# Performance work log

Hardware: AMD Instinct MI355X
Metric: run time of the kernel (lower is better)

## Reference

```python
import jax, jax.numpy as jnp
import numpy as np

N = 50000        # nodes
E_RAND = 800000  # random edges (self-loops appended)
H = 4            # heads
F_IN, D1, D2 = 128, 64, 64
MLP_H, NCLS = 200, 2
NEG_SLOPE = 0.2
EPS = 1e-5


def setup_inputs() -> dict:
    key = jax.random.key(0)
    ks = jax.random.split(key, 18)
    p = lambda k, shape: (jax.random.normal(k, shape, jnp.float32) * 0.05)
    features = jax.random.normal(ks[0], (N, F_IN), jnp.float32)
    loops = jnp.arange(N, dtype=jnp.int32)
    src = jnp.concatenate([jax.random.randint(ks[1], (E_RAND,), 0, N, jnp.int32), loops])
    dst = jnp.concatenate([jax.random.randint(ks[2], (E_RAND,), 0, N, jnp.int32), loops])
    return {
        "features": features, "src": src, "dst": dst,
        "W1": p(ks[3], (F_IN, H * D1)), "al1": p(ks[4], (H, D1)), "ar1": p(ks[5], (H, D1)), "b1": p(ks[6], (H * D1,)),
        "W2": p(ks[7], (D1, H * D2)), "al2": p(ks[8], (H, D2)), "ar2": p(ks[9], (H, D2)), "b2": p(ks[10], (H * D2,)),
        "Wm1": p(ks[11], (D2, MLP_H)), "bm1": p(ks[12], (MLP_H,)),
        "gamma": jnp.ones((MLP_H,), jnp.float32), "beta": jnp.zeros((MLP_H,), jnp.float32),
        "Wm2": p(ks[13], (MLP_H, NCLS)), "bm2": p(ks[14], (NCLS,)),
    }


def gat_layer(x, W, al, ar, b, src, dst):
    # x: [N, F]; W: [F, H*D]
    Hh, D = al.shape
    h = (x @ W).reshape(N, Hh, D)                      # [N,H,D]
    el = jnp.einsum('nhd,hd->nh', h, al)               # [N,H]
    er = jnp.einsum('nhd,hd->nh', h, ar)               # [N,H]
    e = jax.nn.leaky_relu(el[src] + er[dst], NEG_SLOPE)  # [E,H]
    # edge softmax over incoming edges of each dst node
    m = jax.ops.segment_max(e, dst, num_segments=N)    # [N,H]
    ex = jnp.exp(e - m[dst])
    s = jax.ops.segment_sum(ex, dst, num_segments=N)   # [N,H]
    a = ex / s[dst]                                    # [E,H]
    out = jax.ops.segment_sum(a[:, :, None] * h[src], dst, num_segments=N)  # [N,H,D]
    out = jax.nn.relu(out + b.reshape(1, Hh, D))
    return out.mean(axis=1)                            # mean over heads -> [N,D]


def reference(features, src, dst, W1, al1, ar1, b1, W2, al2, ar2, b2,
              Wm1, bm1, gamma, beta, Wm2, bm2):
    h = gat_layer(features, W1, al1, ar1, b1, src, dst)   # dropout = identity (eval)
    h = gat_layer(h, W2, al2, ar2, b2, src, dst)
    # MLPPredictor: Dropout(id) -> Linear -> ReLU -> BatchNorm1d (batch stats) -> Linear
    z = jax.nn.relu(h @ Wm1 + bm1)                        # [N, MLP_H]
    mu = z.mean(axis=0)
    var = ((z - mu) ** 2).mean(axis=0)                    # biased var (torch BN)
    z = (z - mu) * jax.lax.rsqrt(var + EPS) * gamma + beta
    return z @ Wm2 + bm2                                  # [N, NCLS]
```

## Files before the change

### kernel.cpp

```cpp
#include <hip/hip_runtime.h>
#include <hip/hip_bf16.h>

#define NNODES 50000
#define MLP_HID 200
#define NB_SCAN 196
#define CAP 128

#define NB_W1   256
#define NB_W2   256
#define NB_ZC   196
#define INIT_BLOCKS (NB_W1 + NB_W2 + NB_ZC + 1)

typedef __attribute__((ext_vector_type(8))) short bf16x8;
typedef __attribute__((ext_vector_type(4))) float f32x4;

__device__ __forceinline__ unsigned short f2bf(float x){
    unsigned u = __float_as_uint(x);
    unsigned r = (u + 0x7fffu + ((u >> 16) & 1u)) >> 16;
    return (unsigned short)r;
}
__device__ __forceinline__ float bflo(unsigned u){ return __uint_as_float(u << 16); }
__device__ __forceinline__ float bfhi(unsigned u){ return __uint_as_float(u & 0xffff0000u); }

__global__ __launch_bounds__(256) void init_all(
    const float* __restrict__ W1, unsigned short* __restrict__ W1T,
    const float* __restrict__ W2, unsigned short* __restrict__ W2T,
    int* __restrict__ cnt, float* __restrict__ bn_acc )
{
    const int b = blockIdx.x, tid = threadIdx.x;
    if (b < NB_W1){
        int c = b;
        if (tid < 128) W1T[(size_t)c * 128 + tid] = f2bf(W1[(size_t)tid * 256 + c]);
    } else if (b < NB_W1 + NB_W2){
        int c = b - NB_W1;
        if (tid < 64) W2T[(size_t)c * 64 + tid] = f2bf(W2[(size_t)tid * 256 + c]);
    } else if (b < NB_W1 + NB_W2 + NB_ZC){
        int i = (b - NB_W1 - NB_W2) * 256 + tid;
        if (i < NNODES) cnt[i] = 0;
    } else {
        if (tid < 2 * MLP_HID - 256) bn_acc[256 + tid] = 0.f;
        bn_acc[tid] = 0.f;
    }
}

template<int K, bool F32IN>
__global__ __launch_bounds__(256) void mfma_gemm_attn(
    const void* __restrict__ Aptr,
    const unsigned short* __restrict__ WT,
    const float* __restrict__ al, const float* __restrict__ ar,
    unsigned short* __restrict__ hb,
    float* __restrict__ el, float* __restrict__ er, int M)
{
    const int wv = threadIdx.x >> 6, lane = threadIdx.x & 63;
    const int r0 = blockIdx.x * 64 + wv * 16;
    const int l15 = lane & 15, ks = lane >> 4;

    f32x4 acc[16];
    #pragma unroll
    for (int nt = 0; nt < 16; nt++)
        #pragma unroll
        for (int q = 0; q < 4; q++) acc[nt][q] = 0.f;

    const int arow = min(r0 + l15, M - 1);
    const unsigned short* aptr_b = (const unsigned short*)Aptr + (size_t)arow * K + ks * 8;
    const float*          aptr_f = (const float*)Aptr          + (size_t)arow * K + ks * 8;
    const unsigned short* bptr = WT + (size_t)l15 * K + ks * 8;

    #pragma unroll
    for (int k0 = 0; k0 < K; k0 += 32){
        bf16x8 a;
        if (F32IN){
            float4 f0 = *(const float4*)(aptr_f + k0);
            float4 f1 = *(const float4*)(aptr_f + k0 + 4);
            a[0] = (short)f2bf(f0.x); a[1] = (short)f2bf(f0.y);
            a[2] = (short)f2bf(f0.z); a[3] = (short)f2bf(f0.w);
            a[4] = (short)f2bf(f1.x); a[5] = (short)f2bf(f1.y);
            a[6] = (short)f2bf(f1.z); a[7] = (short)f2bf(f1.w);
        } else {
            a = *(const bf16x8*)(aptr_b + k0);
        }
        #pragma unroll
        for (int nt = 0; nt < 16; nt++){
            bf16x8 b = *(const bf16x8*)(bptr + (size_t)nt * 16 * K + k0);
            acc[nt] = __builtin_amdgcn_mfma_f32_16x16x32_bf16(a, b, acc[nt], 0, 0, 0);
        }
    }

    float elv[4][4], erv[4][4];
    #pragma unroll
    for (int r = 0; r < 4; r++)
        #pragma unroll
        for (int hh = 0; hh < 4; hh++){ elv[r][hh] = 0.f; erv[r][hh] = 0.f; }

    #pragma unroll
    for (int nt = 0; nt < 16; nt++){
        int col = nt * 16 + l15;
        float alv = al[col], arv = ar[col];
        #pragma unroll
        for (int reg = 0; reg < 4; reg++){
            elv[reg][nt >> 2] = fmaf(acc[nt][reg], alv, elv[reg][nt >> 2]);
            erv[reg][nt >> 2] = fmaf(acc[nt][reg], arv, erv[reg][nt >> 2]);
        }
    }
    #pragma unroll
    for (int o = 8; o > 0; o >>= 1){
        #pragma unroll
        for (int reg = 0; reg < 4; reg++)
            #pragma unroll
            for (int hh = 0; hh < 4; hh++){
                elv[reg][hh] += __shfl_xor(elv[reg][hh], o);
                erv[reg][hh] += __shfl_xor(erv[reg][hh], o);
            }
    }
    if (l15 == 0){
        #pragma unroll
        for (int reg = 0; reg < 4; reg++){
            int r = r0 + ks * 4 + reg;
            if (r < M){
                #pragma unroll
                for (int hh = 0; hh < 4; hh++){
                    el[r * 4 + hh] = elv[reg][hh];
                    er[r * 4 + hh] = erv[reg][hh];
                }
            }
        }
    }

    __shared__ __align__(16) unsigned short hbuf[4][16][264];
    #pragma unroll
    for (int nt = 0; nt < 16; nt++)
        #pragma unroll
        for (int reg = 0; reg < 4; reg++)
            hbuf[wv][ks * 4 + reg][nt * 16 + l15] = f2bf(acc[nt][reg]);
    #pragma unroll
    for (int t = 0; t < 8; t++){
        int chunk = t * 64 + lane;
        int rr = chunk >> 5;
        int cc = (chunk & 31) * 8;
        int r = r0 + rr;
        if (r < M){
            uint4 v = *(const uint4*)&hbuf[wv][rr][cc];
            *(uint4*)&hb[(size_t)r * 256 + cc] = v;
        }
    }
}

template<int KT, bool RELU, bool BN>
__global__ __launch_bounds__(256) void gemm_tile(const float* __restrict__ A,
                                                 const float* __restrict__ B,
                                                 const float* __restrict__ bias,
                                                 float* __restrict__ C,
                                                 float* __restrict__ bn_sum,
                                                 float* __restrict__ bn_sumsq,
                                                 int M, int Nc){
    __shared__ float As[16][64];
    __shared__ float Bs[16][64];
    __shared__ float bnred[16][64];
    const int tid = threadIdx.x;
    const int tx = tid & 15, ty = tid >> 4;
    const int r0 = blockIdx.y * 64, c0 = blockIdx.x * 64;
    float acc[4][4] = {};
    const int lr  = tid >> 2,  lk4 = (tid & 3) * 4;
    const int bk  = tid >> 4,  bc4 = (tid & 15) * 4;

    for (int k0 = 0; k0 < KT; k0 += 16){
        float4 av = make_float4(0.f,0.f,0.f,0.f);
        if (r0 + lr < M) av = *(const float4*)&A[(size_t)(r0 + lr) * KT + k0 + lk4];
        As[lk4+0][lr] = av.x; As[lk4+1][lr] = av.y;
        As[lk4+2][lr] = av.z; As[lk4+3][lr] = av.w;

        if (c0 + bc4 + 3 < Nc){
            float4 bv = *(const float4*)&B[(size_t)(k0 + bk) * Nc + c0 + bc4];
            Bs[bk][bc4+0] = bv.x; Bs[bk][bc4+1] = bv.y;
            Bs[bk][bc4+2] = bv.z; Bs[bk][bc4+3] = bv.w;
        } else {
            #pragma unroll
            for (int j = 0; j < 4; j++){
                int c = c0 + bc4 + j;
                Bs[bk][bc4+j] = (c < Nc) ? B[(size_t)(k0 + bk) * Nc + c] : 0.f;
            }
        }
        __syncthreads();
        #pragma unroll
        for (int kk = 0; kk < 16; kk++){
            float4 a = *(const float4*)&As[kk][ty*4];
            float4 b = *(const float4*)&Bs[kk][tx*4];
            float arr[4] = {a.x,a.y,a.z,a.w};
            float brr[4] = {b.x,b.y,b.z,b.w};
            #pragma unroll
            for (int i = 0; i < 4; i++)
                #pragma unroll
                for (int j = 0; j < 4; j++)
                    acc[i][j] = fmaf(arr[i], brr[j], acc[i][j]);
        }
        __syncthreads();
    }

    float cs[4] = {0,0,0,0}, css[4] = {0,0,0,0};
    #pragma unroll
    for (int i = 0; i < 4; i++){
        int r = r0 + ty*4 + i;
        bool rok = r < M;
        #pragma unroll
        for (int j = 0; j < 4; j++){
            int c = c0 + tx*4 + j;
            if (c >= Nc) continue;
            float v = acc[i][j];
            if (bias) v += bias[c];
            if (RELU) v = fmaxf(v, 0.f);
            if (rok){
                C[(size_t)r * Nc + c] = v;
                if (BN){ cs[j] += v; css[j] += v * v; }
            }
        }
    }
    if (BN){
        #pragma unroll
        for (int j = 0; j < 4; j++) bnred[ty][tx*4+j] = cs[j];
        __syncthreads();
        if (tid < 64){
            float s = 0.f;
            #pragma unroll
            for (int t = 0; t < 16; t++) s += bnred[t][tid];
            if (c0 + tid < Nc) atomicAdd(&bn_sum[c0 + tid], s);
        }
        __syncthreads();
        #pragma unroll
        for (int j = 0; j < 4; j++) bnred[ty][tx*4+j] = css[j];
        __syncthreads();
        if (tid < 64){
            float s = 0.f;
            #pragma unroll
            for (int t = 0; t < 16; t++) s += bnred[t][tid];
            if (c0 + tid < Nc) atomicAdd(&bn_sumsq[c0 + tid], s);
        }
    }
}

__global__ __launch_bounds__(256) void csr_count(const int* __restrict__ dst,
                                                 int* __restrict__ cnt, int E){
    int e = blockIdx.x * blockDim.x + threadIdx.x;
    if (e < E) atomicAdd(&cnt[dst[e]], 1);
}

__global__ __launch_bounds__(256) void csr_bsum(const int* __restrict__ cnt,
                                                int* __restrict__ bsum){
    __shared__ int red[256];
    int i = blockIdx.x * 256 + threadIdx.x;
    red[threadIdx.x] = (i < NNODES) ? cnt[i] : 0;
    __syncthreads();
    for (int off = 128; off > 0; off >>= 1){
        if (threadIdx.x < off) red[threadIdx.x] += red[threadIdx.x + off];
        __syncthreads();
    }
    if (threadIdx.x == 0) bsum[blockIdx.x] = red[0];
}

__global__ __launch_bounds__(256) void csr_bscan(const int* __restrict__ bsum,
                                                 int* __restrict__ boff){
    __shared__ int part[256];
    int t = threadIdx.x;
    int v = (t < NB_SCAN) ? bsum[t] : 0;
    part[t] = v;
    __syncthreads();
    for (int off = 1; off < 256; off <<= 1){
        int u = (t >= off) ? part[t - off] : 0;
        __syncthreads();
        part[t] += u;
        __syncthreads();
    }
    if (t < NB_SCAN) boff[t] = part[t] - v;
}

__global__ __launch_bounds__(256) void csr_fill(const int* __restrict__ cnt,
                                                const int* __restrict__ boff,
                                                int* __restrict__ row_ptr,
                                                int* __restrict__ cursor){
    __shared__ int part[256];
    int b = blockIdx.x, t = threadIdx.x;
    int i = b * 256 + t;
    int c = (i < NNODES) ? cnt[i] : 0;
    part[t] = c;
    __syncthreads();
    for (int off = 1; off < 256; off <<= 1){
        int u = (t >= off) ? part[t - off] : 0;
        __syncthreads();
        part[t] += u;
        __syncthreads();
    }
    int excl = part[t] - c + boff[b];
    if (i < NNODES){ row_ptr[i] = excl; cursor[i] = excl; }
    if (i == NNODES - 1) row_ptr[NNODES] = excl + c;
}

__global__ __launch_bounds__(256) void csr_scatter(const int* __restrict__ src,
                                                   const int* __restrict__ dst,
                                                   int* __restrict__ cursor,
                                                   int* __restrict__ col_src, int E){
    int e = blockIdx.x * blockDim.x + threadIdx.x;
    if (e >= E) return;
    int pos = atomicAdd(&cursor[dst[e]], 1);
    col_src[pos] = src[e];
}

__global__ __launch_bounds__(256) void gat_edge_v7(
    const int* __restrict__ row_ptr, const int* __restrict__ col_src,
    const float* __restrict__ el, const float* __restrict__ er,
    const unsigned short* __restrict__ hb, const float* __restrict__ bias,
    float* __restrict__ out_f, unsigned short* __restrict__ out_b, int N)
{
    __shared__ float s_w[4][4][132];
    __shared__ int   s_idx[4][CAP];

    const int wv = threadIdx.x >> 6;
    const int lane = threadIdx.x & 63;
    const int n = blockIdx.x * 4 + wv;
    if (n >= N) return;

    const int rs = row_ptr[n], re = row_ptr[n + 1];
    const int K = re - rs;
    const float4 ern = *(const float4*)&er[n * 4];
    float (*sw)[132] = s_w[wv];
    int* sidx = s_idx[wv];

    float ls0 = 0.f, ls1 = 0.f, ls2 = 0.f, ls3 = 0.f;
    for (int k = lane; k < K; k += 64){
        int s = col_src[rs + k];
        float4 e4 = *(const float4*)&el[s * 4];
        float e0 = e4.x + ern.x; e0 = (e0 >= 0.f) ? e0 : 0.2f * e0;
        float e1 = e4.y + ern.y; e1 = (e1 >= 0.f) ? e1 : 0.2f * e1;
        float e2 = e4.z + ern.z; e2 = (e2 >= 0.f) ? e2 : 0.2f * e2;
        float e3 = e4.w + ern.w; e3 = (e3 >= 0.f) ? e3 : 0.2f * e3;
        float w0 = __expf(e0), w1 = __expf(e1), w2 = __expf(e2), w3 = __expf(e3);
        if (k < CAP){
            sidx[k] = s;
            sw[0][k] = w0; sw[1][k] = w1; sw[2][k] = w2; sw[3][k] = w3;
        }
        ls0 += w0; ls1 += w1; ls2 += w2; ls3 += w3;
    }
    #pragma unroll
    for (int o = 32; o > 0; o >>= 1){
        ls0 += __shfl_xor(ls0, o); ls1 += __shfl_xor(ls1, o);
        ls2 += __shfl_xor(ls2, o); ls3 += __shfl_xor(ls3, o);
    }
    const int slot = lane >> 5;
    const int c8   = (lane & 31) * 8;
    const int hc   = c8 >> 6;
    const float invh = 1.f / (hc == 0 ? ls0 : hc == 1 ? ls1 : hc == 2 ? ls2 : ls3);

    float acc[8];
    #pragma unroll
    for (int q = 0; q < 8; q++) acc[q] = 0.f;

    for (int base = 0; base < K; base += CAP){
        if (base > 0){
            for (int k = base + lane; k < min(K, base + CAP); k += 64){
                int s = col_src[rs + k];
                float4 e4 = *(const float4*)&el[s * 4];
                float e0 = e4.x + ern.x; e0 = (e0 >= 0.f) ? e0 : 0.2f * e0;
                float e1 = e4.y + ern.y; e1 = (e1 >= 0.f) ? e1 : 0.2f * e1;
                float e2 = e4.z + ern.z; e2 = (e2 >= 0.f) ? e2 : 0.2f * e2;
                float e3 = e4.w + ern.w; e3 = (e3 >= 0.f) ? e3 : 0.2f * e3;
                int kk = k - base;
                sidx[kk] = s;
                sw[0][kk] = __expf(e0); sw[1][kk] = __expf(e1);
                sw[2][kk] = __expf(e2); sw[3][kk] = __expf(e3);
            }
        }
        const int rem = min(CAP, K - base);
        for (int j = slot; j < rem; j += 8){
            int   j1 = j + 2, j2 = j + 4, j3 = j + 6;
            int   jc1 = min(j1, rem - 1), jc2 = min(j2, rem - 1), jc3 = min(j3, rem - 1);
            float w0v = sw[hc][j];
            float w1v = (j1 < rem) ? sw[hc][j1] : 0.f;
            float w2v = (j2 < rem) ? sw[hc][j2] : 0.f;
            float w3v = (j3 < rem) ? sw[hc][j3] : 0.f;
            int   s0 = sidx[j], s1 = sidx[jc1], s2 = sidx[jc2], s3 = sidx[jc3];
            uint4 v0 = *(const uint4*)&hb[(size_t)s0 * 256 + c8];
            uint4 v1 = *(const uint4*)&hb[(size_t)s1 * 256 + c8];
            uint4 v2 = *(const uint4*)&hb[(size_t)s2 * 256 + c8];
            uint4 v3 = *(const uint4*)&hb[(size_t)s3 * 256 + c8];
            acc[0] = fmaf(w0v, bflo(v0.x), acc[0]); acc[1] = fmaf(w0v, bfhi(v0.x), acc[1]);
            acc[2] = fmaf(w0v, bflo(v0.y), acc[2]); acc[3] = fmaf(w0v, bfhi(v0.y), acc[3]);
            acc[4] = fmaf(w0v, bflo(v0.z), acc[4]); acc[5] = fmaf(w0v, bfhi(v0.z), acc[5]);
            acc[6] = fmaf(w0v, bflo(v0.w), acc[6]); acc[7] = fmaf(w0v, bfhi(v0.w), acc[7]);
            acc[0] = fmaf(w1v, bflo(v1.x), acc[0]); acc[1] = fmaf(w1v, bfhi(v1.x), acc[1]);
            acc[2] = fmaf(w1v, bflo(v1.y), acc[2]); acc[3] = fmaf(w1v, bfhi(v1.y), acc[3]);
            acc[4] = fmaf(w1v, bflo(v1.z), acc[4]); acc[5] = fmaf(w1v, bfhi(v1.z), acc[5]);
            acc[6] = fmaf(w1v, bflo(v1.w), acc[6]); acc[7] = fmaf(w1v, bfhi(v1.w), acc[7]);
            acc[0] = fmaf(w2v, bflo(v2.x), acc[0]); acc[1] = fmaf(w2v, bfhi(v2.x), acc[1]);
            acc[2] = fmaf(w2v, bflo(v2.y), acc[2]); acc[3] = fmaf(w2v, bfhi(v2.y), acc[3]);
            acc[4] = fmaf(w2v, bflo(v2.z), acc[4]); acc[5] = fmaf(w2v, bfhi(v2.z), acc[5]);
            acc[6] = fmaf(w2v, bflo(v2.w), acc[6]); acc[7] = fmaf(w2v, bfhi(v2.w), acc[7]);
            acc[0] = fmaf(w3v, bflo(v3.x), acc[0]); acc[1] = fmaf(w3v, bfhi(v3.x), acc[1]);
            acc[2] = fmaf(w3v, bflo(v3.y), acc[2]); acc[3] = fmaf(w3v, bfhi(v3.y), acc[3]);
            acc[4] = fmaf(w3v, bflo(v3.z), acc[4]); acc[5] = fmaf(w3v, bfhi(v3.z), acc[5]);
            acc[6] = fmaf(w3v, bflo(v3.w), acc[6]); acc[7] = fmaf(w3v, bfhi(v3.w), acc[7]);
        }
    }

    #pragma unroll
    for (int q = 0; q < 8; q++){
        acc[q] *= invh;
        acc[q] += __shfl_xor(acc[q], 32);
        acc[q] = fmaxf(acc[q] + bias[c8 + q], 0.f);
        acc[q] += __shfl_xor(acc[q], 8);
        acc[q] += __shfl_xor(acc[q], 16);
        acc[q] *= 0.25f;
    }
    if (lane < 8){
        uint4 pb;
        pb.x = (unsigned)f2bf(acc[0]) | ((unsigned)f2bf(acc[1]) << 16);
        pb.y = (unsigned)f2bf(acc[2]) | ((unsigned)f2bf(acc[3]) << 16);
        pb.z = (unsigned)f2bf(acc[4]) | ((unsigned)f2bf(acc[5]) << 16);
        pb.w = (unsigned)f2bf(acc[6]) | ((unsigned)f2bf(acc[7]) << 16);
        *(uint4*)&out_b[(size_t)n * 64 + lane * 8] = pb;
        if (out_f){
            *(float4*)&out_f[(size_t)n * 64 + lane * 8]     = make_float4(acc[0], acc[1], acc[2], acc[3]);
            *(float4*)&out_f[(size_t)n * 64 + lane * 8 + 4] = make_float4(acc[4], acc[5], acc[6], acc[7]);
        }
    }
}

__global__ __launch_bounds__(256) void mlp2(const float* __restrict__ z,
                                            const float* __restrict__ bn_sum,
                                            const float* __restrict__ bn_sumsq,
                                            const float* __restrict__ gamma,
                                            const float* __restrict__ beta,
                                            const float* __restrict__ Wm2,
                                            const float* __restrict__ bm2,
                                            float* __restrict__ out,
                                            int Nrows){
    __shared__ float s_scale[MLP_HID], s_shift[MLP_HID];
    const int tid = threadIdx.x;
    if (tid < MLP_HID){
        float inv = 1.f / (float)Nrows;
        float mu = bn_sum[tid] * inv;
        float var = bn_sumsq[tid] * inv - mu * mu;
        float rstd = rsqrtf(var + 1e-5f);
        float sc = rstd * gamma[tid];
        s_scale[tid] = sc;
        s_shift[tid] = beta[tid] - mu * sc;
    }
    __syncthreads();
    int n = (blockIdx.x * 256 + tid) >> 6;
    if (n >= Nrows) return;
    int lane = tid & 63;
    float a0 = 0.f, a1 = 0.f;
    for (int k = lane; k < MLP_HID; k += 64){
        float zn = z[(size_t)n * MLP_HID + k] * s_scale[k] + s_shift[k];
        a0 = fmaf(zn, Wm2[k * 2 + 0], a0);
        a1 = fmaf(zn, Wm2[k * 2 + 1], a1);
    }
    #pragma unroll
    for (int o = 32; o > 0; o >>= 1){
        a0 += __shfl_xor(a0, o);
        a1 += __shfl_xor(a1, o);
    }
    if (lane == 0){
        out[n * 2 + 0] = a0 + bm2[0];
        out[n * 2 + 1] = a1 + bm2[1];
    }
}

extern "C" void kernel_launch(void* const* d_in, const int* in_sizes, int n_in,
                              void* d_out, int out_size, void* d_ws, size_t ws_size,
                              hipStream_t stream) {
    const float* feat  = (const float*)d_in[0];
    const int*   src   = (const int*)  d_in[1];
    const int*   dst   = (const int*)  d_in[2];
    const float* W1    = (const float*)d_in[3];
    const float* al1   = (const float*)d_in[4];
    const float* ar1   = (const float*)d_in[5];
    const float* b1    = (const float*)d_in[6];
    const float* W2    = (const float*)d_in[7];
    const float* al2   = (const float*)d_in[8];
    const float* ar2   = (const float*)d_in[9];
    const float* b2    = (const float*)d_in[10];
    const float* Wm1   = (const float*)d_in[11];
    const float* bm1   = (const float*)d_in[12];
    const float* gamma = (const float*)d_in[13];
    const float* beta  = (const float*)d_in[14];
    const float* Wm2   = (const float*)d_in[15];
    const float* bm2   = (const float*)d_in[16];
    const int E = in_sizes[1];
    float* out = (float*)d_out;

    unsigned short* h_bf   = (unsigned short*)d_ws;
    unsigned short* o1_bf  = h_bf   + (size_t)NNODES * 256;
    unsigned short* o2_bf  = o1_bf  + (size_t)NNODES * 64;
    unsigned short* W1T    = o2_bf  + (size_t)NNODES * 64;
    unsigned short* W2T    = W1T + 256 * 128;
    float* z      = (float*)(W2T + 256 * 64);
    float* out2_f = z      + (size_t)NNODES * MLP_HID;
    float* el     = out2_f + (size_t)NNODES * 64;
    float* er     = el     + (size_t)NNODES * 4;
    float* bn_sum   = er + (size_t)NNODES * 4;
    float* bn_sumsq = bn_sum + MLP_HID;
    int* cnt      = (int*)(bn_sumsq + MLP_HID);
    int* row_ptr  = cnt + NNODES;
    int* cursor   = row_ptr + NNODES + 1;
    int* bsum     = cursor + NNODES;
    int* boff     = bsum + 256;
    int* col_src  = boff + 256;

    const dim3 blk(256);
    const int eg = (E + 255) / 256;
    const int gb = (NNODES + 63) / 64;
    const int ng4 = (NNODES + 3) / 4;

    init_all<<<INIT_BLOCKS, blk, 0, stream>>>(W1, W1T, W2, W2T, cnt, bn_sum);

    csr_count<<<eg, blk, 0, stream>>>(dst, cnt, E);
    csr_bsum<<<NB_SCAN, blk, 0, stream>>>(cnt, bsum);
    csr_bscan<<<1, blk, 0, stream>>>(bsum, boff);
    csr_fill<<<NB_SCAN, blk, 0, stream>>>(cnt, boff, row_ptr, cursor);
    csr_scatter<<<eg, blk, 0, stream>>>(src, dst, cursor, col_src, E);

    mfma_gemm_attn<128, true><<<gb, blk, 0, stream>>>(feat, W1T, al1, ar1,
                                                      h_bf, el, er, NNODES);
    gat_edge_v7<<<ng4, blk, 0, stream>>>(row_ptr, col_src, el, er, h_bf, b1,
                                         nullptr, o1_bf, NNODES);

    mfma_gemm_attn<64, false><<<gb, blk, 0, stream>>>(o1_bf, W2T, al2, ar2,
                                                      h_bf, el, er, NNODES);
    gat_edge_v7<<<ng4, blk, 0, stream>>>(row_ptr, col_src, el, er, h_bf, b2,
                                         out2_f, o2_bf, NNODES);

    gemm_tile<64,true,true><<<dim3((MLP_HID + 63) / 64, gb), blk, 0, stream>>>(
        out2_f, Wm1, bm1, z, bn_sum, bn_sumsq, NNODES, MLP_HID);

    mlp2<<<(NNODES * 64 + 255) / 256, blk, 0, stream>>>(
        z, bn_sum, bn_sumsq, gamma, beta, Wm2, bm2, out, NNODES);
}
```

Measured before the change: 372.3 us.

## Split GAT edge kernel into weight pass and slab-sliced aggregation

The GEMM now writes node features into eight 64-byte feature slabs, each holding 8 dims across all heads, instead of 512-byte rows. Edge aggregation is split in two. A weight kernel precomputes normalized softmax weights per edge as packed bf16 and writes them to a new buffer. A slab kernel then gathers from one slice per block, so the gathered working set per pass is smaller and more cache-friendly. In exchange it adds an extra kernel launch and an edge-weight array write/read per layer, re-reads col_src eight times, and rounds the attention weights to bf16.

```diff
diff --git a/kernel.cpp b/kernel.cpp
--- a/kernel.cpp
+++ b/kernel.cpp
@@ -48,7 +48,7 @@
     const void* __restrict__ Aptr,
     const unsigned short* __restrict__ WT,
     const float* __restrict__ al, const float* __restrict__ ar,
-    unsigned short* __restrict__ hb,
+    unsigned short* __restrict__ hslab,
     float* __restrict__ el, float* __restrict__ er, int M)
 {
     const int wv = threadIdx.x >> 6, lane = threadIdx.x & 63;
@@ -139,8 +139,11 @@
         int cc = (chunk & 31) * 8;
         int r = r0 + rr;
         if (r < M){
+            int hh = cc >> 6;
+            int d0 = cc & 63;
+            int s  = d0 >> 3;
             uint4 v = *(const uint4*)&hbuf[wv][rr][cc];
-            *(uint4*)&hb[(size_t)r * 256 + cc] = v;
+            *(uint4*)&hslab[((size_t)s * NNODES + r) * 32 + hh * 8] = v;
         }
     }
 }
@@ -303,15 +306,12 @@
     col_src[pos] = src[e];
 }
 
-__global__ __launch_bounds__(256) void gat_edge_v7(
+__global__ __launch_bounds__(256) void gat_edge_wts(
     const int* __restrict__ row_ptr, const int* __restrict__ col_src,
     const float* __restrict__ el, const float* __restrict__ er,
-    const unsigned short* __restrict__ hb, const float* __restrict__ bias,
-    float* __restrict__ out_f, unsigned short* __restrict__ out_b, int N)
+    uint2* __restrict__ apack, int N)
 {
     __shared__ float s_w[4][4][132];
-    __shared__ int   s_idx[4][CAP];
-
     const int wv = threadIdx.x >> 6;
     const int lane = threadIdx.x & 63;
     const int n = blockIdx.x * 4 + wv;
@@ -321,7 +321,6 @@
     const int K = re - rs;
     const float4 ern = *(const float4*)&er[n * 4];
     float (*sw)[132] = s_w[wv];
-    int* sidx = s_idx[wv];
 
     float ls0 = 0.f, ls1 = 0.f, ls2 = 0.f, ls3 = 0.f;
     for (int k = lane; k < K; k += 64){
@@ -333,7 +332,6 @@
         float e3 = e4.w + ern.w; e3 = (e3 >= 0.f) ? e3 : 0.2f * e3;
         float w0 = __expf(e0), w1 = __expf(e1), w2 = __expf(e2), w3 = __expf(e3);
         if (k < CAP){
-            sidx[k] = s;
             sw[0][k] = w0; sw[1][k] = w1; sw[2][k] = w2; sw[3][k] = w3;
         }
         ls0 += w0; ls1 += w1; ls2 += w2; ls3 += w3;
@@ -343,81 +341,83 @@
         ls0 += __shfl_xor(ls0, o); ls1 += __shfl_xor(ls1, o);
         ls2 += __shfl_xor(ls2, o); ls3 += __shfl_xor(ls3, o);
     }
-    const int slot = lane >> 5;
-    const int c8   = (lane & 31) * 8;
-    const int hc   = c8 >> 6;
-    const float invh = 1.f / (hc == 0 ? ls0 : hc == 1 ? ls1 : hc == 2 ? ls2 : ls3);
+    const float i0 = 1.f / ls0, i1 = 1.f / ls1, i2 = 1.f / ls2, i3 = 1.f / ls3;
+
+    for (int k = lane; k < K; k += 64){
+        float w0, w1, w2, w3;
+        if (k < CAP){
+            w0 = sw[0][k]; w1 = sw[1][k]; w2 = sw[2][k]; w3 = sw[3][k];
+        } else {
+            int s = col_src[rs + k];
+            float4 e4 = *(const float4*)&el[s * 4];
+            float e0 = e4.x + ern.x; e0 = (e0 >= 0.f) ? e0 : 0.2f * e0;
+            float e1 = e4.y + ern.y; e1 = (e1 >= 0.f) ? e1 : 0.2f * e1;
+            float e2 = e4.z + ern.z; e2 = (e2 >= 0.f) ? e2 : 0.2f * e2;
+            float e3 = e4.w + ern.w; e3 = (e3 >= 0.f) ? e3 : 0.2f * e3;
+            w0 = __expf(e0); w1 = __expf(e1); w2 = __expf(e2); w3 = __expf(e3);
+        }
+        uint2 ap;
+        ap.x = (unsigned)f2bf(w0 * i0) | ((unsigned)f2bf(w1 * i1) << 16);
+        ap.y = (unsigned)f2bf(w2 * i2) | ((unsigned)f2bf(w3 * i3) << 16);
+        apack[rs + k] = ap;
+    }
+}
+
+__global__ __launch_bounds__(256) void gat_edge_slab(
+    const int* __restrict__ row_ptr, const int* __restrict__ col_src,
+    const uint2* __restrict__ apack, const unsigned short* __restrict__ hslab,
+    const float* __restrict__ bias,
+    float* __restrict__ out_f, unsigned short* __restrict__ out_b, int N)
+{
+    const int slice = blockIdx.x & 7;
+    const int n = (blockIdx.x >> 3) * 8 + (threadIdx.x >> 5);
+    if (n >= N) return;
+    const int l32 = threadIdx.x & 31;
+    const int slot = l32 >> 2, ht = l32 & 3;
+    const int rs = row_ptr[n], re = row_ptr[n + 1];
+    const int K = re - rs;
+    const unsigned short* base = hslab + (size_t)slice * NNODES * 32 + ht * 8;
 
     float acc[8];
     #pragma unroll
     for (int q = 0; q < 8; q++) acc[q] = 0.f;
 
-    for (int base = 0; base < K; base += CAP){
-        if (base > 0){
-            for (int k = base + lane; k < min(K, base + CAP); k += 64){
-                int s = col_src[rs + k];
-                float4 e4 = *(const float4*)&el[s * 4];
-                float e0 = e4.x + ern.x; e0 = (e0 >= 0.f) ? e0 : 0.2f * e0;
-                float e1 = e4.y + ern.y; e1 = (e1 >= 0.f) ? e1 : 0.2f * e1;
-                float e2 = e4.z + ern.z; e2 = (e2 >= 0.f) ? e2 : 0.2f * e2;
-                float e3 = e4.w + ern.w; e3 = (e3 >= 0.f) ? e3 : 0.2f * e3;
-                int kk = k - base;
-                sidx[kk] = s;
-                sw[0][kk] = __expf(e0); sw[1][kk] = __expf(e1);
-                sw[2][kk] = __expf(e2); sw[3][kk] = __expf(e3);
-            }
-        }
-        const int rem = min(CAP, K - base);
-        for (int j = slot; j < rem; j += 8){
-            int   j1 = j + 2, j2 = j + 4, j3 = j + 6;
-            int   jc1 = min(j1, rem - 1), jc2 = min(j2, rem - 1), jc3 = min(j3, rem - 1);
-            float w0v = sw[hc][j];
-            float w1v = (j1 < rem) ? sw[hc][j1] : 0.f;
-            float w2v = (j2 < rem) ? sw[hc][j2] : 0.f;
-            float w3v = (j3 < rem) ? sw[hc][j3] : 0.f;
-            int   s0 = sidx[j], s1 = sidx[jc1], s2 = sidx[jc2], s3 = sidx[jc3];
-            uint4 v0 = *(const uint4*)&hb[(size_t)s0 * 256 + c8];
-            uint4 v1 = *(const uint4*)&hb[(size_t)s1 * 256 + c8];
-            uint4 v2 = *(const uint4*)&hb[(size_t)s2 * 256 + c8];
-            uint4 v3 = *(const uint4*)&hb[(size_t)s3 * 256 + c8];
-            acc[0] = fmaf(w0v, bflo(v0.x), acc[0]); acc[1] = fmaf(w0v, bfhi(v0.x), acc[1]);
-            acc[2] = fmaf(w0v, bflo(v0.y), acc[2]); acc[3] = fmaf(w0v, bfhi(v0.y), acc[3]);
-            acc[4] = fmaf(w0v, bflo(v0.z), acc[4]); acc[5] = fmaf(w0v, bfhi(v0.z), acc[5]);
-            acc[6] = fmaf(w0v, bflo(v0.w), acc[6]); acc[7] = fmaf(w0v, bfhi(v0.w), acc[7]);
-            acc[0] = fmaf(w1v, bflo(v1.x), acc[0]); acc[1] = fmaf(w1v, bfhi(v1.x), acc[1]);
-            acc[2] = fmaf(w1v, bflo(v1.y), acc[2]); acc[3] = fmaf(w1v, bfhi(v1.y), acc[3]);
-            acc[4] = fmaf(w1v, bflo(v1.z), acc[4]); acc[5] = fmaf(w1v, bfhi(v1.z), acc[5]);
-            acc[6] = fmaf(w1v, bflo(v1.w), acc[6]); acc[7] = fmaf(w1v, bfhi(v1.w), acc[7]);
-            acc[0] = fmaf(w2v, bflo(v2.x), acc[0]); acc[1] = fmaf(w2v, bfhi(v2.x), acc[1]);
-            acc[2] = fmaf(w2v, bflo(v2.y), acc[2]); acc[3] = fmaf(w2v, bfhi(v2.y), acc[3]);
-            acc[4] = fmaf(w2v, bflo(v2.z), acc[4]); acc[5] = fmaf(w2v, bfhi(v2.z), acc[5]);
-            acc[6] = fmaf(w2v, bflo(v2.w), acc[6]); acc[7] = fmaf(w2v, bfhi(v2.w), acc[7]);
-            acc[0] = fmaf(w3v, bflo(v3.x), acc[0]); acc[1] = fmaf(w3v, bfhi(v3.x), acc[1]);
-            acc[2] = fmaf(w3v, bflo(v3.y), acc[2]); acc[3] = fmaf(w3v, bfhi(v3.y), acc[3]);
-            acc[4] = fmaf(w3v, bflo(v3.z), acc[4]); acc[5] = fmaf(w3v, bfhi(v3.z), acc[5]);
-            acc[6] = fmaf(w3v, bflo(v3.w), acc[6]); acc[7] = fmaf(w3v, bfhi(v3.w), acc[7]);
-        }
+    for (int k = slot; k < K; k += 8){
+        int idx = col_src[rs + k];
+        uint2 ap = apack[rs + k];
+        unsigned wsel = (ht & 2) ? ap.y : ap.x;
+        float w = (ht & 1) ? bfhi(wsel) : bflo(wsel);
+        uint4 v = *(const uint4*)&base[(size_t)idx * 32];
+        acc[0] = fmaf(w, bflo(v.x), acc[0]); acc[1] = fmaf(w, bfhi(v.x), acc[1]);
+        acc[2] = fmaf(w, bflo(v.y), acc[2]); acc[3] = fmaf(w, bfhi(v.y), acc[3]);
+        acc[4] = fmaf(w, bflo(v.z), acc[4]); acc[5] = fmaf(w, bfhi(v.z), acc[5]);
+        acc[6] = fmaf(w, bflo(v.w), acc[6]); acc[7] = fmaf(w, bfhi(v.w), acc[7]);
     }
 
     #pragma unroll
     for (int q = 0; q < 8; q++){
-        acc[q] *= invh;
-        acc[q] += __shfl_xor(acc[q], 32);
-        acc[q] = fmaxf(acc[q] + bias[c8 + q], 0.f);
+        acc[q] += __shfl_xor(acc[q], 4);
         acc[q] += __shfl_xor(acc[q], 8);
         acc[q] += __shfl_xor(acc[q], 16);
+    }
+    const int d0 = slice * 8;
+    #pragma unroll
+    for (int q = 0; q < 8; q++){
+        acc[q] = fmaxf(acc[q] + bias[ht * 64 + d0 + q], 0.f);
+        acc[q] += __shfl_xor(acc[q], 1);
+        acc[q] += __shfl_xor(acc[q], 2);
         acc[q] *= 0.25f;
     }
-    if (lane < 8){
+    if (l32 == 0){
         uint4 pb;
         pb.x = (unsigned)f2bf(acc[0]) | ((unsigned)f2bf(acc[1]) << 16);
         pb.y = (unsigned)f2bf(acc[2]) | ((unsigned)f2bf(acc[3]) << 16);
         pb.z = (unsigned)f2bf(acc[4]) | ((unsigned)f2bf(acc[5]) << 16);
         pb.w = (unsigned)f2bf(acc[6]) | ((unsigned)f2bf(acc[7]) << 16);
-        *(uint4*)&out_b[(size_t)n * 64 + lane * 8] = pb;
+        *(uint4*)&out_b[(size_t)n * 64 + d0] = pb;
         if (out_f){
-            *(float4*)&out_f[(size_t)n * 64 + lane * 8]     = make_float4(acc[0], acc[1], acc[2], acc[3]);
-            *(float4*)&out_f[(size_t)n * 64 + lane * 8 + 4] = make_float4(acc[4], acc[5], acc[6], acc[7]);
+            *(float4*)&out_f[(size_t)n * 64 + d0]     = make_float4(acc[0], acc[1], acc[2], acc[3]);
+            *(float4*)&out_f[(size_t)n * 64 + d0 + 4] = make_float4(acc[4], acc[5], acc[6], acc[7]);
         }
     }
 }
@@ -486,8 +486,8 @@
     const int E = in_sizes[1];
     float* out = (float*)d_out;
 
-    unsigned short* h_bf   = (unsigned short*)d_ws;
-    unsigned short* o1_bf  = h_bf   + (size_t)NNODES * 256;
+    unsigned short* hslab  = (unsigned short*)d_ws;
+    unsigned short* o1_bf  = hslab  + (size_t)NNODES * 256;
     unsigned short* o2_bf  = o1_bf  + (size_t)NNODES * 64;
     unsigned short* W1T    = o2_bf  + (size_t)NNODES * 64;
     unsigned short* W2T    = W1T + 256 * 128;
@@ -503,11 +503,13 @@
     int* bsum     = cursor + NNODES;
     int* boff     = bsum + 256;
     int* col_src  = boff + 256;
+    uint2* apack  = (uint2*)(col_src + E + (E & 1));
 
     const dim3 blk(256);
     const int eg = (E + 255) / 256;
     const int gb = (NNODES + 63) / 64;
     const int ng4 = (NNODES + 3) / 4;
+    const int ngs = ((NNODES + 7) / 8) * 8;
 
     init_all<<<INIT_BLOCKS, blk, 0, stream>>>(W1, W1T, W2, W2T, cnt, bn_sum);
 
@@ -518,14 +520,16 @@
     csr_scatter<<<eg, blk, 0, stream>>>(src, dst, cursor, col_src, E);
 
     mfma_gemm_attn<128, true><<<gb, blk, 0, stream>>>(feat, W1T, al1, ar1,
-                                                      h_bf, el, er, NNODES);
-    gat_edge_v7<<<ng4, blk, 0, stream>>>(row_ptr, col_src, el, er, h_bf, b1,
-                                         nullptr, o1_bf, NNODES);
+                                                      hslab, el, er, NNODES);
+    gat_edge_wts<<<ng4, blk, 0, stream>>>(row_ptr, col_src, el, er, apack, NNODES);
+    gat_edge_slab<<<ngs, blk, 0, stream>>>(row_ptr, col_src, apack, hslab, b1,
+                                           nullptr, o1_bf, NNODES);
 
     mfma_gemm_attn<64, false><<<gb, blk, 0, stream>>>(o1_bf, W2T, al2, ar2,
-                                                      h_bf, el, er, NNODES);
-    gat_edge_v7<<<ng4, blk, 0, stream>>>(row_ptr, col_src, el, er, h_bf, b2,
-                                         out2_f, o2_bf, NNODES);
+                                                      hslab, el, er, NNODES);
+    gat_edge_wts<<<ng4, blk, 0, stream>>>(row_ptr, col_src, el, er, apack, NNODES);
+    gat_edge_slab<<<ngs, blk, 0, stream>>>(row_ptr, col_src, apack, hslab, b2,
+                                           out2_f, o2_bf, NNODES);
 
     gemm_tile<64,true,true><<<dim3((MLP_HID + 63) / 64, gb), blk, 0, stream>>>(
         out2_f, Wm1, bm1, z, bn_sum, bn_sumsq, NNODES, MLP_HID);
```

Result: slower. 496.4 us (+33.3%).

## Aggregate layer-2 inputs before projecting with W2 to shrink gathered rows

Applied to the files above, without the earlier changes.

Layer 2 now uses linearity to reorder the work. Per-head attention aggregation is applied to the 64-wide bf16 layer-1 output instead of the 256-wide projected h, and the W2 projection then runs per head on the aggregated result, followed by bias, ReLU and the head mean. The layer-2 GEMM kernel only computes el/er and no longer stores h. This cuts the gathered bytes per edge by 4x. In exchange it adds an extra MFMA kernel and a 256-wide per-node intermediate, and the edge kernel holds 32 accumulators per lane instead of 8.

```diff
diff --git a/kernel.cpp b/kernel.cpp
--- a/kernel.cpp
+++ b/kernel.cpp
@@ -43,7 +43,7 @@
     }
 }
 
-template<int K, bool F32IN>
+template<int K, bool F32IN, bool STOREH>
 __global__ __launch_bounds__(256) void mfma_gemm_attn(
     const void* __restrict__ Aptr,
     const unsigned short* __restrict__ WT,
@@ -126,21 +126,84 @@
         }
     }
 
-    __shared__ __align__(16) unsigned short hbuf[4][16][264];
-    #pragma unroll
-    for (int nt = 0; nt < 16; nt++)
-        #pragma unroll
-        for (int reg = 0; reg < 4; reg++)
-            hbuf[wv][ks * 4 + reg][nt * 16 + l15] = f2bf(acc[nt][reg]);
-    #pragma unroll
-    for (int t = 0; t < 8; t++){
+    if constexpr (STOREH){
+        __shared__ __align__(16) unsigned short hbuf[4][16][264];
+        #pragma unroll
+        for (int nt = 0; nt < 16; nt++)
+            #pragma unroll
+            for (int reg = 0; reg < 4; reg++)
+                hbuf[wv][ks * 4 + reg][nt * 16 + l15] = f2bf(acc[nt][reg]);
+        #pragma unroll
+        for (int t = 0; t < 8; t++){
+            int chunk = t * 64 + lane;
+            int rr = chunk >> 5;
+            int cc = (chunk & 31) * 8;
+            int r = r0 + rr;
+            if (r < M){
+                uint4 v = *(const uint4*)&hbuf[wv][rr][cc];
+                *(uint4*)&hb[(size_t)r * 256 + cc] = v;
+            }
+        }
+    }
+}
+
+__global__ __launch_bounds__(256) void mfma_apply_w2(
+    const unsigned short* __restrict__ agg2,
+    const unsigned short* __restrict__ W2T,
+    const float* __restrict__ b2,
+    float* __restrict__ out_f, unsigned short* __restrict__ out_b, int M)
+{
+    const int wv = threadIdx.x >> 6, lane = threadIdx.x & 63;
+    const int r0 = blockIdx.x * 64 + wv * 16;
+    const int l15 = lane & 15, ks = lane >> 4;
+    const int arow = min(r0 + l15, M - 1);
+
+    f32x4 acc[4][4];
+    #pragma unroll
+    for (int h = 0; h < 4; h++)
+        #pragma unroll
+        for (int nt = 0; nt < 4; nt++)
+            #pragma unroll
+            for (int q = 0; q < 4; q++) acc[h][nt][q] = 0.f;
+
+    #pragma unroll
+    for (int k0 = 0; k0 < 64; k0 += 32){
+        #pragma unroll
+        for (int h = 0; h < 4; h++){
+            bf16x8 a = *(const bf16x8*)&agg2[(size_t)arow * 256 + h * 64 + ks * 8 + k0];
+            #pragma unroll
+            for (int nt = 0; nt < 4; nt++){
+                bf16x8 b = *(const bf16x8*)&W2T[(size_t)(h * 64 + nt * 16 + l15) * 64 + ks * 8 + k0];
+                acc[h][nt] = __builtin_amdgcn_mfma_f32_16x16x32_bf16(a, b, acc[h][nt], 0, 0, 0);
+            }
+        }
+    }
+
+    __shared__ __align__(16) float obuf[4][16][68];
+    #pragma unroll
+    for (int nt = 0; nt < 4; nt++){
+        #pragma unroll
+        for (int reg = 0; reg < 4; reg++){
+            float s = 0.f;
+            #pragma unroll
+            for (int h = 0; h < 4; h++)
+                s += fmaxf(acc[h][nt][reg] + b2[h * 64 + nt * 16 + l15], 0.f);
+            obuf[wv][ks * 4 + reg][nt * 16 + l15] = s * 0.25f;
+        }
+    }
+    #pragma unroll
+    for (int t = 0; t < 4; t++){
         int chunk = t * 64 + lane;
-        int rr = chunk >> 5;
-        int cc = (chunk & 31) * 8;
+        int rr = chunk >> 4;
+        int cc = (chunk & 15) * 4;
         int r = r0 + rr;
         if (r < M){
-            uint4 v = *(const uint4*)&hbuf[wv][rr][cc];
-            *(uint4*)&hb[(size_t)r * 256 + cc] = v;
+            float4 v = *(const float4*)&obuf[wv][rr][cc];
+            *(float4*)&out_f[(size_t)r * 64 + cc] = v;
+            uint2 pb;
+            pb.x = (unsigned)f2bf(v.x) | ((unsigned)f2bf(v.y) << 16);
+            pb.y = (unsigned)f2bf(v.z) | ((unsigned)f2bf(v.w) << 16);
+            *(uint2*)&out_b[(size_t)r * 64 + cc] = pb;
         }
     }
 }
@@ -307,7 +370,7 @@
     const int* __restrict__ row_ptr, const int* __restrict__ col_src,
     const float* __restrict__ el, const float* __restrict__ er,
     const unsigned short* __restrict__ hb, const float* __restrict__ bias,
-    float* __restrict__ out_f, unsigned short* __restrict__ out_b, int N)
+    unsigned short* __restrict__ out_b, int N)
 {
     __shared__ float s_w[4][4][132];
     __shared__ int   s_idx[4][CAP];
@@ -415,9 +478,117 @@
         pb.z = (unsigned)f2bf(acc[4]) | ((unsigned)f2bf(acc[5]) << 16);
         pb.w = (unsigned)f2bf(acc[6]) | ((unsigned)f2bf(acc[7]) << 16);
         *(uint4*)&out_b[(size_t)n * 64 + lane * 8] = pb;
-        if (out_f){
-            *(float4*)&out_f[(size_t)n * 64 + lane * 8]     = make_float4(acc[0], acc[1], acc[2], acc[3]);
-            *(float4*)&out_f[(size_t)n * 64 + lane * 8 + 4] = make_float4(acc[4], acc[5], acc[6], acc[7]);
+    }
+}
+
+__global__ __launch_bounds__(256) void gat_edge_agg(
+    const int* __restrict__ row_ptr, const int* __restrict__ col_src,
+    const float* __restrict__ el, const float* __restrict__ er,
+    const unsigned short* __restrict__ o1, unsigned short* __restrict__ agg2, int N)
+{
+    __shared__ float s_w[4][4][132];
+    __shared__ int   s_idx[4][CAP];
+
+    const int wv = threadIdx.x >> 6;
+    const int lane = threadIdx.x & 63;
+    const int n = blockIdx.x * 4 + wv;
+    if (n >= N) return;
+
+    const int rs = row_ptr[n], re = row_ptr[n + 1];
+    const int K = re - rs;
+    const float4 ern = *(const float4*)&er[n * 4];
+    float (*sw)[132] = s_w[wv];
+    int* sidx = s_idx[wv];
+
+    float ls0 = 0.f, ls1 = 0.f, ls2 = 0.f, ls3 = 0.f;
+    for (int k = lane; k < K; k += 64){
+        int s = col_src[rs + k];
+        float4 e4 = *(const float4*)&el[s * 4];
+        float e0 = e4.x + ern.x; e0 = (e0 >= 0.f) ? e0 : 0.2f * e0;
+        float e1 = e4.y + ern.y; e1 = (e1 >= 0.f) ? e1 : 0.2f * e1;
+        float e2 = e4.z + ern.z; e2 = (e2 >= 0.f) ? e2 : 0.2f * e2;
+        float e3 = e4.w + ern.w; e3 = (e3 >= 0.f) ? e3 : 0.2f * e3;
+        float w0 = __expf(e0), w1 = __expf(e1), w2 = __expf(e2), w3 = __expf(e3);
+        if (k < CAP){
+            sidx[k] = s;
+            sw[0][k] = w0; sw[1][k] = w1; sw[2][k] = w2; sw[3][k] = w3;
+        }
+        ls0 += w0; ls1 += w1; ls2 += w2; ls3 += w3;
+    }
+    #pragma unroll
+    for (int o = 32; o > 0; o >>= 1){
+        ls0 += __shfl_xor(ls0, o); ls1 += __shfl_xor(ls1, o);
+        ls2 += __shfl_xor(ls2, o); ls3 += __shfl_xor(ls3, o);
+    }
+
+    const int slot = lane >> 3;
+    const int c8   = (lane & 7) * 8;
+    float acc[4][8];
+    #pragma unroll
+    for (int h = 0; h < 4; h++)
+        #pragma unroll
+        for (int q = 0; q < 8; q++) acc[h][q] = 0.f;
+
+    for (int base = 0; base < K; base += CAP){
+        if (base > 0){
+            for (int k = base + lane; k < min(K, base + CAP); k += 64){
+                int s = col_src[rs + k];
+                float4 e4 = *(const float4*)&el[s * 4];
+                float e0 = e4.x + ern.x; e0 = (e0 >= 0.f) ? e0 : 0.2f * e0;
+                float e1 = e4.y + ern.y; e1 = (e1 >= 0.f) ? e1 : 0.2f * e1;
+                float e2 = e4.z + ern.z; e2 = (e2 >= 0.f) ? e2 : 0.2f * e2;
+                float e3 = e4.w + ern.w; e3 = (e3 >= 0.f) ? e3 : 0.2f * e3;
+                int kk = k - base;
+                sidx[kk] = s;
+                sw[0][kk] = __expf(e0); sw[1][kk] = __expf(e1);
+                sw[2][kk] = __expf(e2); sw[3][kk] = __expf(e3);
+            }
+        }
+        const int rem = min(CAP, K - base);
+        for (int j = slot; j < rem; j += 8){
+            int sN = sidx[j];
+            float w0 = sw[0][j], w1 = sw[1][j], w2 = sw[2][j], w3 = sw[3][j];
+            uint4 v = *(const uint4*)&o1[(size_t)sN * 64 + c8];
+            float f0 = bflo(v.x), f1 = bfhi(v.x), f2 = bflo(v.y), f3 = bfhi(v.y);
+            float f4 = bflo(v.z), f5 = bfhi(v.z), f6 = bflo(v.w), f7 = bfhi(v.w);
+            acc[0][0] = fmaf(w0, f0, acc[0][0]); acc[0][1] = fmaf(w0, f1, acc[0][1]);
+            acc[0][2] = fmaf(w0, f2, acc[0][2]); acc[0][3] = fmaf(w0, f3, acc[0][3]);
+            acc[0][4] = fmaf(w0, f4, acc[0][4]); acc[0][5] = fmaf(w0, f5, acc[0][5]);
+            acc[0][6] = fmaf(w0, f6, acc[0][6]); acc[0][7] = fmaf(w0, f7, acc[0][7]);
+            acc[1][0] = fmaf(w1, f0, acc[1][0]); acc[1][1] = fmaf(w1, f1, acc[1][1]);
+            acc[1][2] = fmaf(w1, f2, acc[1][2]); acc[1][3] = fmaf(w1, f3, acc[1][3]);
+            acc[1][4] = fmaf(w1, f4, acc[1][4]); acc[1][5] = fmaf(w1, f5, acc[1][5]);
+            acc[1][6] = fmaf(w1, f6, acc[1][6]); acc[1][7] = fmaf(w1, f7, acc[1][7]);
+            acc[2][0] = fmaf(w2, f0, acc[2][0]); acc[2][1] = fmaf(w2, f1, acc[2][1]);
+            acc[2][2] = fmaf(w2, f2, acc[2][2]); acc[2][3] = fmaf(w2, f3, acc[2][3]);
+            acc[2][4] = fmaf(w2, f4, acc[2][4]); acc[2][5] = fmaf(w2, f5, acc[2][5]);
+            acc[2][6] = fmaf(w2, f6, acc[2][6]); acc[2][7] = fmaf(w2, f7, acc[2][7]);
+            acc[3][0] = fmaf(w3, f0, acc[3][0]); acc[3][1] = fmaf(w3, f1, acc[3][1]);
+            acc[3][2] = fmaf(w3, f2, acc[3][2]); acc[3][3] = fmaf(w3, f3, acc[3][3]);
+            acc[3][4] = fmaf(w3, f4, acc[3][4]); acc[3][5] = fmaf(w3, f5, acc[3][5]);
+            acc[3][6] = fmaf(w3, f6, acc[3][6]); acc[3][7] = fmaf(w3, f7, acc[3][7]);
+        }
+    }
+
+    #pragma unroll
+    for (int h = 0; h < 4; h++)
+        #pragma unroll
+        for (int q = 0; q < 8; q++){
+            acc[h][q] += __shfl_xor(acc[h][q], 8);
+            acc[h][q] += __shfl_xor(acc[h][q], 16);
+            acc[h][q] += __shfl_xor(acc[h][q], 32);
+        }
+
+    if (lane < 8){
+        const float inv[4] = {1.f / ls0, 1.f / ls1, 1.f / ls2, 1.f / ls3};
+        #pragma unroll
+        for (int h = 0; h < 4; h++){
+            uint4 pb;
+            pb.x = (unsigned)f2bf(acc[h][0] * inv[h]) | ((unsigned)f2bf(acc[h][1] * inv[h]) << 16);
+            pb.y = (unsigned)f2bf(acc[h][2] * inv[h]) | ((unsigned)f2bf(acc[h][3] * inv[h]) << 16);
+            pb.z = (unsigned)f2bf(acc[h][4] * inv[h]) | ((unsigned)f2bf(acc[h][5] * inv[h]) << 16);
+            pb.w = (unsigned)f2bf(acc[h][6] * inv[h]) | ((unsigned)f2bf(acc[h][7] * inv[h]) << 16);
+            *(uint4*)&agg2[(size_t)n * 256 + h * 64 + c8] = pb;
         }
     }
 }
@@ -503,6 +674,7 @@
     int* bsum     = cursor + NNODES;
     int* boff     = bsum + 256;
     int* col_src  = boff + 256;
+    unsigned short* agg2 = h_bf;
 
     const dim3 blk(256);
     const int eg = (E + 255) / 256;
@@ -517,15 +689,16 @@
     csr_fill<<<NB_SCAN, blk, 0, stream>>>(cnt, boff, row_ptr, cursor);
     csr_scatter<<<eg, blk, 0, stream>>>(src, dst, cursor, col_src, E);
 
-    mfma_gemm_attn<128, true><<<gb, blk, 0, stream>>>(feat, W1T, al1, ar1,
-                                                      h_bf, el, er, NNODES);
+    mfma_gemm_attn<128, true, true><<<gb, blk, 0, stream>>>(
+        feat, W1T, al1, ar1, h_bf, el, er, NNODES);
     gat_edge_v7<<<ng4, blk, 0, stream>>>(row_ptr, col_src, el, er, h_bf, b1,
-                                         nullptr, o1_bf, NNODES);
-
-    mfma_gemm_attn<64, false><<<gb, blk, 0, stream>>>(o1_bf, W2T, al2, ar2,
-                                                      h_bf, el, er, NNODES);
-    gat_edge_v7<<<ng4, blk, 0, stream>>>(row_ptr, col_src, el, er, h_bf, b2,
-                                         out2_f, o2_bf, NNODES);
+                                         o1_bf, NNODES);
+
+    mfma_gemm_attn<64, false, false><<<gb, blk, 0, stream>>>(
+        o1_bf, W2T, al2, ar2, nullptr, el, er, NNODES);
+    gat_edge_agg<<<ng4, blk, 0, stream>>>(row_ptr, col_src, el, er,
+                                          o1_bf, agg2, NNODES);
+    mfma_apply_w2<<<gb, blk, 0, stream>>>(agg2, W2T, b2, out2_f, o2_bf, NNODES);
 
     gemm_tile<64,true,true><<<dim3((MLP_HID + 63) / 64, gb), blk, 0, stream>>>(
         out2_f, Wm1, bm1, z, bn_sum, bn_sumsq, NNODES, MLP_HID);
```

New measurement: 388.5 us. 4.3% more time.
